# Kernel optimization log

Measured on AMD Instinct MI355X. Metric: run time of the kernel, lower is better.

The kernel has to match this reference:

```python
import jax, jax.numpy as jnp
import numpy as np

N = 1_000_000      # neurons (scaled-up NEURON_COUNT)
E = 20_000_000     # synapses (scaled-up NEURON_COUNT * SYNAPSE_RATIO)
IN = 4096          # input_size
OUT = 4096         # output_size
STEPS = 3


def setup_inputs() -> dict:
    key = jax.random.key(0)
    k1, k2, k3, k4, k5 = jax.random.split(key, 5)
    x = jax.random.normal(k1, (IN,), jnp.float32)
    synapse_src = jax.random.randint(k2, (E,), 0, N)
    synapse_dst = jax.random.randint(k3, (E,), 0, N)
    synapse_weights = jax.random.normal(k4, (E,), jnp.float32)
    neuron_biases = jax.random.normal(k5, (N - IN,), jnp.float32)
    input_indices = jnp.arange(IN)              # first IN neurons are inputs
    output_indices = jnp.arange(N - OUT, N)     # last OUT neurons are outputs
    non_input_indices = jnp.arange(IN, N)       # complement of input_indices
    return {
        "x": x,
        "synapse_weights": synapse_weights,
        "neuron_biases": neuron_biases,
        "synapse_src": synapse_src,
        "synapse_dst": synapse_dst,
        "input_indices": input_indices,
        "output_indices": output_indices,
        "non_input_indices": non_input_indices,
    }


def reference(x, synapse_weights, neuron_biases, synapse_src, synapse_dst,
              input_indices, output_indices, non_input_indices):
    # out_mask[i] True => neuron i is an output (skipped by tanh)
    out_mask = jnp.zeros(N, dtype=bool).at[output_indices].set(True)
    # initial state: zeros with inputs written in
    v = jnp.zeros(N, dtype=x.dtype).at[input_indices].set(x)
    for _ in range(STEPS):
        # per-edge multiply + scatter-add into destination neurons
        msgs = v[synapse_src] * synapse_weights          # [E]
        nxt = jax.ops.segment_sum(msgs, synapse_dst, num_segments=N)  # [N]
        # bias only for non-input neurons
        nxt = nxt.at[non_input_indices].add(neuron_biases)
        # tanh everywhere except output neurons
        v = jnp.where(out_mask, nxt, jnp.tanh(nxt))
    return v[output_indices]
```

## Files before the change

kernel.cpp:

```cpp
#include <hip/hip_runtime.h>

#define THREADS 256
#define BTHREADS 1024
#define SCTHREADS 1024
#define BSHIFT 11
#define BSIZE 2048
#define NBMAX 512
#define PASS_EDGES 8192
#define EPT 8
#define G 4
#define GSHIFT 2
#define ACCSIZE 8192
#define SPLIT 4
#define NPSMAX 640
typedef unsigned int u32;
typedef unsigned short u16;
typedef unsigned long long u64;


__global__ void prep_kernel(const float* __restrict__ x, const float* __restrict__ bias,
                            float* __restrict__ v, float* __restrict__ nxt,
                            int N, int IN) {
    int i = blockIdx.x * THREADS + threadIdx.x;
    if (i >= N) return;
    v[i]   = (i < IN) ? x[i] : 0.0f;
    nxt[i] = (i < IN) ? 0.0f : bias[i - IN];
}

__global__ void finalize0_kernel(float* __restrict__ v, int N, int OUT) {
    int i = blockIdx.x * THREADS + threadIdx.x;
    if (i >= N) return;
    float val = v[i];
    v[i] = (i >= N - OUT) ? val : tanhf(val);
}

__global__ void finalize_fast_kernel(float* __restrict__ nxt, const float* __restrict__ bias,
                                     float* __restrict__ out,
                                     int N, int IN, int OUT) {
    int i = blockIdx.x * THREADS + threadIdx.x;
    if (i >= N) return;
    float val = nxt[i] + (i >= IN ? bias[i - IN] : 0.0f);
    bool isOut = (i >= N - OUT);
    float a = isOut ? val : tanhf(val);
    nxt[i] = a;
    if (out != nullptr && isOut) out[i - (N - OUT)] = a;
}

__global__ void __launch_bounds__(SCTHREADS)
scatter_kernel(const int* __restrict__ src, const int* __restrict__ dst,
               const float* __restrict__ w,
               const float* __restrict__ vA,
               float* __restrict__ vB,
               uint2* __restrict__ e8, u16* __restrict__ dir,
               int E, int IN, int NB, int NP) {
    __shared__ uint2 stage[PASS_EDGES];
    __shared__ u32 hc[NBMAX];
    __shared__ u32 runStart[NBMAX + 1];

    const int tid = threadIdx.x;
    for (int i = tid; i < NBMAX; i += SCTHREADS) hc[i] = 0;
    __syncthreads();

    for (int p = blockIdx.x; p < NP; p += gridDim.x) {
        int ps = p * PASS_EDGES;
        int pe = ps + PASS_EDGES; if (pe > E) pe = E;
        int cntAll = pe - ps;

        int base = ps + tid * EPT;
        u32 pk[EPT]; u32 bk[EPT]; u32 wb[EPT];
        int cnt = 0;
        if (base + EPT <= pe) {
            int4 s0 = *(const int4*)(src + base), s1 = *(const int4*)(src + base + 4);
            int4 d0 = *(const int4*)(dst + base), d1 = *(const int4*)(dst + base + 4);
            float4 w0 = *(const float4*)(w + base), w1 = *(const float4*)(w + base + 4);
            int ss[EPT] = {s0.x, s0.y, s0.z, s0.w, s1.x, s1.y, s1.z, s1.w};
            int dd[EPT] = {d0.x, d0.y, d0.z, d0.w, d1.x, d1.y, d1.z, d1.w};
            float ww[EPT] = {w0.x, w0.y, w0.z, w0.w, w1.x, w1.y, w1.z, w1.w};
            cnt = EPT;
            #pragma unroll
            for (int i = 0; i < EPT; ++i) {
                u32 d = (u32)dd[i];
                bk[i] = d >> BSHIFT;
                pk[i] = (u32)ss[i] | ((d & (BSIZE - 1u)) << 20);
                wb[i] = __float_as_uint(ww[i]);
                if (ss[i] < IN) atomicAdd(&vB[dd[i]], vA[ss[i]] * ww[i]);
            }
        } else {
            for (int i = 0; i < EPT; ++i) {
                int e = base + i;
                if (e < pe) {
                    int s = src[e];
                    u32 d = (u32)dst[e];
                    float wv = w[e];
                    bk[cnt] = d >> BSHIFT;
                    pk[cnt] = (u32)s | ((d & (BSIZE - 1u)) << 20);
                    wb[cnt] = __float_as_uint(wv);
                    if (s < IN) atomicAdd(&vB[d], vA[s] * wv);
                    ++cnt;
                }
            }
        }

        for (int i = 0; i < cnt; ++i) atomicAdd(&hc[bk[i]], 1u);
        __syncthreads();

        if (tid < 64) {
            u32 c[8]; u32 s = 0;
            #pragma unroll
            for (int k = 0; k < 8; ++k) { c[k] = hc[tid * 8 + k]; s += c[k]; }
            u32 inc = s;
            #pragma unroll
            for (int off = 1; off < 64; off <<= 1) {
                u32 t = __shfl_up(inc, off, 64);
                if (tid >= off) inc += t;
            }
            u32 excl = inc - s;
            #pragma unroll
            for (int k = 0; k < 8; ++k) {
                runStart[tid * 8 + k] = excl;
                excl += c[k];
                hc[tid * 8 + k] = 0;
            }
            if (tid == 63) runStart[NBMAX] = excl;
        }
        __syncthreads();

        for (int i = 0; i < cnt; ++i) {
            u32 b = bk[i];
            u32 r = atomicAdd(&hc[b], 1u);
            stage[runStart[b] + r] = make_uint2(pk[i], wb[i]);
        }
        __syncthreads();

        for (int j = tid * 2; j + 1 < cntAll; j += SCTHREADS * 2)
            *(uint4*)(e8 + ps + j) = *(const uint4*)(stage + j);
        if ((cntAll & 1) && tid == 0) e8[ps + cntAll - 1] = stage[cntAll - 1];
        if (tid <= NB) dir[(u32)p * (u32)(NB + 1) + tid] = (u16)runStart[tid];
        if (tid < NBMAX) hc[tid] = 0;
        __syncthreads();
    }
}

__global__ void __launch_bounds__(BTHREADS)
bucket_step_kernel(const uint2* __restrict__ e8, const u16* __restrict__ dir,
                   const float* __restrict__ v_in, float* __restrict__ nxt,
                   int N, int NB, int NP) {
    __shared__ float acc[ACCSIZE];
    __shared__ u16 sb[G + 1][NPSMAX];
    const int tid = threadIdx.x;
    const int gb = blockIdx.x >> 2;
    const int sp = blockIdx.x & 3;

    const int NPS = (NP + SPLIT - 1) / SPLIT;
    const int p0 = sp * NPS;
    int pc = NP - p0; if (pc > NPS) pc = NPS; if (pc < 0) pc = 0;

    const int b0 = gb << GSHIFT;
    for (int idx = tid; idx < pc * (G + 1); idx += BTHREADS) {
        int i = idx / (G + 1), k = idx - i * (G + 1);
        int col = b0 + k; if (col > NB) col = NB;
        sb[k][i] = dir[(u32)(p0 + i) * (u32)(NB + 1) + col];
    }
    for (int i = tid; i < ACCSIZE; i += BTHREADS) acc[i] = 0.0f;
    __syncthreads();

    const int wv = tid >> 6, ln = tid & 63;
    for (int pp = wv; pp < pc; pp += 64) {
        int  jj[4], je[4], eb[4];
        u32  s1[4], s2[4], s3[4];
        bool act[4];
        #pragma unroll
        for (int c = 0; c < 4; ++c) {
            int i = pp + c * 16;
            act[c] = false;
            if (i < pc) {
                u32 a0 = sb[0][i];
                s1[c] = sb[1][i]; s2[c] = sb[2][i]; s3[c] = sb[3][i];
                jj[c] = (int)a0 + ln;
                je[c] = (int)sb[4][i];
                eb[c] = (p0 + i) * PASS_EDGES;
                act[c] = jj[c] < je[c];
            }
        }
        while (act[0] | act[1] | act[2] | act[3]) {
            u64 pv[4];
            #pragma unroll
            for (int c = 0; c < 4; ++c)
                if (act[c]) pv[c] = __builtin_nontemporal_load((const u64*)(e8 + eb[c] + jj[c]));
            float vv[4];
            #pragma unroll
            for (int c = 0; c < 4; ++c)
                if (act[c]) vv[c] = v_in[(u32)pv[c] & 0xFFFFFu];
            #pragma unroll
            for (int c = 0; c < 4; ++c) {
                if (act[c]) {
                    u32 px = (u32)pv[c];
                    u32 j  = (u32)jj[c];
                    u32 r  = (u32)(j >= s1[c]) + (u32)(j >= s2[c]) + (u32)(j >= s3[c]);
                    float pw = __uint_as_float((u32)(pv[c] >> 32));
                    atomicAdd(&acc[(r << BSHIFT) + (px >> 20)], vv[c] * pw);
                    jj[c] += 64;
                    act[c] = jj[c] < je[c];
                }
            }
        }
    }
    __syncthreads();

    int nbase = b0 << BSHIFT;
    for (int j = tid; j < ACCSIZE; j += BTHREADS) {
        int idx = nbase + j;
        if (idx < N) atomicAdd(&nxt[idx], acc[j]);
    }
}


__global__ void edge_kernel(const int* __restrict__ src, const int* __restrict__ dst,
                            const float* __restrict__ w, const float* __restrict__ v,
                            float* __restrict__ nxt, int E) {
    int k = blockIdx.x * THREADS + threadIdx.x;
    int E4 = E >> 2;
    if (k < E4) {
        int4 s = ((const int4*)src)[k];
        int4 d = ((const int4*)dst)[k];
        float4 wv = ((const float4*)w)[k];
        atomicAdd(&nxt[d.x], v[s.x] * wv.x);
        atomicAdd(&nxt[d.y], v[s.y] * wv.y);
        atomicAdd(&nxt[d.z], v[s.z] * wv.z);
        atomicAdd(&nxt[d.w], v[s.w] * wv.w);
    }
    if (k == 0) {
        for (int e = E4 << 2; e < E; ++e)
            atomicAdd(&nxt[dst[e]], v[src[e]] * w[e]);
    }
}

__global__ void finalize_kernel(float* __restrict__ nxt, float* __restrict__ v,
                                const float* __restrict__ bias, float* __restrict__ out,
                                int N, int IN, int OUT) {
    int i = blockIdx.x * THREADS + threadIdx.x;
    if (i >= N) return;
    float val = nxt[i];
    bool isOut = (i >= N - OUT);
    float a = isOut ? val : tanhf(val);
    v[i] = a;
    nxt[i] = (i < IN) ? 0.0f : bias[i - IN];
    if (out != nullptr && isOut) out[i - (N - OUT)] = a;
}


extern "C" void kernel_launch(void* const* d_in, const int* in_sizes, int n_in,
                              void* d_out, int out_size, void* d_ws, size_t ws_size,
                              hipStream_t stream) {
    const float* x    = (const float*)d_in[0];
    const float* w    = (const float*)d_in[1];
    const float* bias = (const float*)d_in[2];
    const int* src = (const int*)d_in[3];
    const int* dst = (const int*)d_in[4];

    const int IN  = in_sizes[0];
    const int E   = in_sizes[1];
    const int N   = IN + in_sizes[2];
    const int OUT = out_size;

    const int NP = (E + PASS_EDGES - 1) / PASS_EDGES;
    const int NB = (N + BSIZE - 1) >> BSHIFT;

    uint2* e8   = (uint2*)d_ws;
    u16*   dir  = (u16*)(e8 + E);
    size_t dirB = (size_t)NP * (size_t)(NB + 1) * sizeof(u16);
    float* vA   = (float*)((char*)dir + ((dirB + 15) & ~(size_t)15));
    float* vB   = vA + N;
    size_t need = (size_t)((char*)(vB + N) - (char*)d_ws);

    int nBlocks = (N + THREADS - 1) / THREADS;

    if (ws_size >= need && N <= (NBMAX << BSHIFT) && NP <= SPLIT * NPSMAX) {
        const int NBG = ((NB + G - 1) >> GSHIFT);
        prep_kernel<<<nBlocks, THREADS, 0, stream>>>(x, bias, vA, vB, N, IN);
        scatter_kernel<<<512, SCTHREADS, 0, stream>>>(
            src, dst, w, vA, vB, e8, dir, E, IN, NB, NP);
        finalize0_kernel<<<nBlocks, THREADS, 0, stream>>>(vB, N, OUT);
        hipMemsetAsync(vA, 0, (size_t)N * sizeof(float), stream);
        bucket_step_kernel<<<NBG * SPLIT, BTHREADS, 0, stream>>>(
            e8, dir, vB, vA, N, NB, NP);
        finalize_fast_kernel<<<nBlocks, THREADS, 0, stream>>>(vA, bias, nullptr, N, IN, OUT);
        hipMemsetAsync(vB, 0, (size_t)N * sizeof(float), stream);
        bucket_step_kernel<<<NBG * SPLIT, BTHREADS, 0, stream>>>(
            e8, dir, vA, vB, N, NB, NP);
        finalize_fast_kernel<<<nBlocks, THREADS, 0, stream>>>(vB, bias, (float*)d_out, N, IN, OUT);
    } else {
        float* v   = (float*)d_ws;
        float* nxt = v + N;
        int eBlocks = ((E >> 2) + THREADS - 1) / THREADS;
        prep_kernel<<<nBlocks, THREADS, 0, stream>>>(x, bias, v, nxt, N, IN);
        for (int step = 0; step < 3; ++step) {
            edge_kernel<<<eBlocks, THREADS, 0, stream>>>(src, dst, w, v, nxt, E);
            float* outp = (step == 2) ? (float*)d_out : nullptr;
            finalize_kernel<<<nBlocks, THREADS, 0, stream>>>(nxt, v, bias, outp, N, IN, OUT);
        }
    }
}
```

Before: 667.1 us.

## Regroup bucketed edges by source tile so consume steps gather from LDS

```diff
diff --git a/kernel.cpp b/kernel.cpp
--- a/kernel.cpp
+++ b/kernel.cpp
@@ -1,15 +1,21 @@
 #include <hip/hip_runtime.h>
 
 #define THREADS 256
-#define BTHREADS 1024
 #define SCTHREADS 1024
 #define BSHIFT 11
 #define BSIZE 2048
 #define NBMAX 512
 #define PASS_EDGES 8192
 #define EPT 8
+#define GSH 13
+#define GRP 8192
 #define G 4
-#define GSHIFT 2
+#define TSH 13
+#define NTILE 128
+#define SLAB 8192
+#define NPQMAX 640
+#define NUMAX 512
+#define BTHREADS 1024
 #define ACCSIZE 8192
 #define SPLIT 4
 #define NPSMAX 640
@@ -46,6 +52,7 @@
     if (out != nullptr && isOut) out[i - (N - OUT)] = a;
 }
 
+
 __global__ void __launch_bounds__(SCTHREADS)
 scatter_kernel(const int* __restrict__ src, const int* __restrict__ dst,
                const float* __restrict__ w,
@@ -53,7 +60,7 @@
                float* __restrict__ vB,
                uint2* __restrict__ e8, u16* __restrict__ dir,
                int E, int IN, int NB, int NP) {
-    __shared__ uint2 stage[PASS_EDGES];
+    __shared__ __align__(16) uint2 stage[PASS_EDGES];
     __shared__ u32 hc[NBMAX];
     __shared__ u32 runStart[NBMAX + 1];
 
@@ -141,6 +148,238 @@
     }
 }
 
+
+__global__ void unitcnt_kernel(const u16* __restrict__ dir1, u32* __restrict__ mc,
+                               int NB, int NP) {
+    __shared__ u32 wsum[4];
+    const int tid = threadIdx.x;
+    const int g = blockIdx.x >> 2, pq = blockIdx.x & 3;
+    const int NPQ = (NP + 3) >> 2;
+    const int p0 = pq * NPQ;
+    int pc = NP - p0; if (pc > NPQ) pc = NPQ; if (pc < 0) pc = 0;
+    int c0 = g * G; if (c0 > NB) c0 = NB;
+    int c1 = g * G + G; if (c1 > NB) c1 = NB;
+    u32 sum = 0;
+    for (int p = tid; p < pc; p += 256) {
+        const u16* row = dir1 + (u32)(p0 + p) * (u32)(NB + 1);
+        sum += (u32)row[c1] - (u32)row[c0];
+    }
+    #pragma unroll
+    for (int off = 32; off; off >>= 1) sum += __shfl_down(sum, off, 64);
+    if ((tid & 63) == 0) wsum[tid >> 6] = sum;
+    __syncthreads();
+    if (tid == 0) mc[blockIdx.x] = wsum[0] + wsum[1] + wsum[2] + wsum[3];
+}
+
+__global__ void unitscan_kernel(const u32* __restrict__ mc, u32* __restrict__ mo,
+                                u32* __restrict__ mr, int NU) {
+    __shared__ u32 s[NUMAX];
+    const int t = threadIdx.x;
+    u32 cnt = (t < NU) ? mc[t] : 0u;
+    u32 pcnt = (cnt + 1u) & ~1u;
+    s[t] = pcnt;
+    __syncthreads();
+    for (int off = 1; off < NUMAX; off <<= 1) {
+        u32 v = (t >= off) ? s[t - off] : 0u;
+        __syncthreads();
+        s[t] += v;
+        __syncthreads();
+    }
+    if (t < NU) mo[t] = s[t] - pcnt;
+    __syncthreads();
+    u32 rows = (cnt + SLAB - 1u) >> 13;
+    s[t] = rows;
+    __syncthreads();
+    for (int off = 1; off < NUMAX; off <<= 1) {
+        u32 v = (t >= off) ? s[t - off] : 0u;
+        __syncthreads();
+        s[t] += v;
+        __syncthreads();
+    }
+    if (t < NU) mr[t] = s[t] - rows;
+}
+
+__global__ void __launch_bounds__(1024)
+regroup_kernel(const uint2* __restrict__ e8, const u16* __restrict__ dir1,
+               const u32* __restrict__ mo, const u32* __restrict__ mr,
+               uint2* __restrict__ e9, u16* __restrict__ dir2,
+               int NB, int NP) {
+    __shared__ __align__(16) uint2 stg[SLAB];
+    __shared__ u16 sb[G + 1][NPQMAX];
+    __shared__ u32 gpfx[NPQMAX + 1];
+    __shared__ u32 scanb[1024];
+    __shared__ u32 hist[NTILE];
+    __shared__ u32 rs2[NTILE + 1];
+    __shared__ int shr[2];
+
+    const int tid = threadIdx.x, wv = tid >> 6, ln = tid & 63;
+    const int g = blockIdx.x >> 2, pq = blockIdx.x & 3;
+    const int b0 = g * G;
+    const int NPQ = (NP + 3) >> 2;
+    const int p0 = pq * NPQ;
+    int pc = NP - p0; if (pc > NPQ) pc = NPQ; if (pc < 0) pc = 0;
+
+    for (int idx = tid; idx < pc * (G + 1); idx += 1024) {
+        int i = idx / (G + 1), k = idx - i * (G + 1);
+        int col = b0 + k; if (col > NB) col = NB;
+        sb[k][i] = dir1[(u32)(p0 + i) * (u32)(NB + 1) + col];
+    }
+    __syncthreads();
+    u32 own = (tid < pc) ? (u32)sb[G][tid] - (u32)sb[0][tid] : 0u;
+    scanb[tid] = own;
+    __syncthreads();
+    for (int off = 1; off < 1024; off <<= 1) {
+        u32 t = (tid >= off) ? scanb[tid - off] : 0u;
+        __syncthreads();
+        scanb[tid] += t;
+        __syncthreads();
+    }
+    if (tid < pc) gpfx[tid] = scanb[tid] - own;
+    if (tid == 0) gpfx[pc] = (pc > 0) ? scanb[pc - 1] : 0u;
+    __syncthreads();
+
+    const u32 cnt = gpfx[pc];
+    const u32 offU = mo[blockIdx.x];
+    const u32 rowB = mr[blockIdx.x];
+    const int nslab = (int)((cnt + SLAB - 1u) >> 13);
+
+    for (int q = 0; q < nslab; ++q) {
+        const u32 lo = (u32)q << 13;
+        u32 hi = lo + SLAB; if (hi > cnt) hi = cnt;
+        if (tid == 0) {
+            int pl = (q == 0) ? 0 : shr[0];
+            while (pl < pc && gpfx[pl + 1] <= lo) ++pl;
+            int ph = pl;
+            while (ph < pc && gpfx[ph] < hi) ++ph;
+            shr[0] = pl; shr[1] = ph;
+        }
+        if (tid < NTILE) hist[tid] = 0;
+        __syncthreads();
+        const int plo = shr[0], phi = shr[1];
+
+        for (int p = plo + wv; p < phi; p += 16) {
+            const u32 gp = gpfx[p], L = gpfx[p + 1] - gp;
+            const u32 s0 = sb[0][p];
+            const size_t eb = (size_t)(p0 + p) * PASS_EDGES + s0;
+            u32 k0 = (lo > gp) ? lo - gp : 0u;
+            u32 k1 = (hi < gp + L) ? hi - gp : L;
+            for (u32 k = k0 + ln; k < k1; k += 64) {
+                u32 pk = e8[eb + k].x;
+                atomicAdd(&hist[(pk & 0xFFFFFu) >> TSH], 1u);
+            }
+        }
+        __syncthreads();
+        if (tid < 64) {
+            u32 c0 = hist[tid * 2], c1 = hist[tid * 2 + 1];
+            u32 s = c0 + c1, inc = s;
+            #pragma unroll
+            for (int off = 1; off < 64; off <<= 1) {
+                u32 t = __shfl_up(inc, off, 64);
+                if (tid >= off) inc += t;
+            }
+            u32 excl = inc - s;
+            rs2[tid * 2] = excl;
+            rs2[tid * 2 + 1] = excl + c0;
+            hist[tid * 2] = 0; hist[tid * 2 + 1] = 0;
+            if (tid == 63) rs2[NTILE] = inc;
+        }
+        __syncthreads();
+        for (int p = plo + wv; p < phi; p += 16) {
+            const u32 gp = gpfx[p], L = gpfx[p + 1] - gp;
+            const u32 s0 = sb[0][p];
+            const u32 b1 = (u32)sb[1][p] - s0, b2 = (u32)sb[2][p] - s0, b3 = (u32)sb[3][p] - s0;
+            const size_t eb = (size_t)(p0 + p) * PASS_EDGES + s0;
+            u32 k0 = (lo > gp) ? lo - gp : 0u;
+            u32 k1 = (hi < gp + L) ? hi - gp : L;
+            for (u32 k = k0 + ln; k < k1; k += 64) {
+                uint2 rec = e8[eb + k];
+                u32 srcg = rec.x & 0xFFFFFu;
+                u32 dl = rec.x >> 20;
+                u32 r = (u32)(k >= b1) + (u32)(k >= b2) + (u32)(k >= b3);
+                u32 tile = srcg >> TSH;
+                u32 rk = atomicAdd(&hist[tile], 1u);
+                stg[rs2[tile] + rk] =
+                    make_uint2((srcg & (GRP - 1u)) | (((r << BSHIFT) | dl) << TSH), rec.y);
+            }
+        }
+        __syncthreads();
+        const u32 m = hi - lo;
+        u64* o64 = (u64*)(e9 + (size_t)offU + ((size_t)q << 13));
+        const u64* s64 = (const u64*)stg;
+        for (u32 j = tid; j < m; j += 1024)
+            __builtin_nontemporal_store(s64[j], o64 + j);
+        if (tid <= NTILE)
+            dir2[(size_t)(rowB + q) * (NTILE + 1) + tid] = (u16)rs2[tid];
+        __syncthreads();
+    }
+}
+
+__global__ void __launch_bounds__(1024)
+consume_kernel(const uint2* __restrict__ e9, const u16* __restrict__ dir2,
+               const u32* __restrict__ mc, const u32* __restrict__ mo,
+               const u32* __restrict__ mr,
+               const float* __restrict__ v_in, float* __restrict__ nxt,
+               int N) {
+    __shared__ float acc[GRP];
+    __shared__ float vt[GRP];
+    __shared__ u32 uoff[4], urow[4], pfx[5];
+
+    const int tid = threadIdx.x, wv = tid >> 6, ln = tid & 63;
+    const int g = blockIdx.x >> 2, sq = blockIdx.x & 3;
+
+    if (tid < 4) {
+        int u = g * 4 + tid;
+        uoff[tid] = mo[u];
+        urow[tid] = mr[u];
+    }
+    __syncthreads();
+    if (tid == 0) {
+        pfx[0] = 0;
+        for (int i = 0; i < 4; ++i) {
+            u32 c = mc[g * 4 + i];
+            pfx[i + 1] = pfx[i] + ((c + SLAB - 1u) >> 13);
+        }
+    }
+    for (int i = tid; i < GRP; i += 1024) acc[i] = 0.0f;
+    __syncthreads();
+    const int tot = (int)pfx[4];
+
+    for (int s = sq * (NTILE / 4); s < (sq + 1) * (NTILE / 4); ++s) {
+        const int vb = s << TSH;
+        if (vb + GRP <= N) {
+            for (int j = tid; j < GRP / 4; j += 1024)
+                *(float4*)&vt[j * 4] = *(const float4*)(v_in + vb + j * 4);
+        } else {
+            for (int j = tid; j < GRP; j += 1024) {
+                int idx = vb + j;
+                vt[j] = (idx < N) ? v_in[idx] : 0.0f;
+            }
+        }
+        __syncthreads();
+        for (int pr = wv; pr < tot; pr += 16) {
+            int u = 0;
+            while (pr >= (int)pfx[u + 1]) ++u;
+            const int q = pr - (int)pfx[u];
+            const u16* row = dir2 + (size_t)(urow[u] + q) * (NTILE + 1) + s;
+            const u32 a = row[0], b = row[1];
+            const uint2* base = e9 + (size_t)uoff[u] + ((size_t)q << 13);
+            for (u32 j = a + ln; j < b; j += 64) {
+                u64 pv = __builtin_nontemporal_load((const u64*)(base + j));
+                u32 px = (u32)pv;
+                float pw = __uint_as_float((u32)(pv >> 32));
+                atomicAdd(&acc[px >> TSH], vt[px & (GRP - 1u)] * pw);
+            }
+        }
+        __syncthreads();
+    }
+    const int nb = g << GSH;
+    for (int j = tid; j < GRP; j += 1024) {
+        int idx = nb + j;
+        if (idx < N) atomicAdd(&nxt[idx], acc[j]);
+    }
+}
+
+
 __global__ void __launch_bounds__(BTHREADS)
 bucket_step_kernel(const uint2* __restrict__ e8, const u16* __restrict__ dir,
                    const float* __restrict__ v_in, float* __restrict__ nxt,
@@ -155,7 +394,7 @@
     const int p0 = sp * NPS;
     int pc = NP - p0; if (pc > NPS) pc = NPS; if (pc < 0) pc = 0;
 
-    const int b0 = gb << GSHIFT;
+    const int b0 = gb << 2;
     for (int idx = tid; idx < pc * (G + 1); idx += BTHREADS) {
         int i = idx / (G + 1), k = idx - i * (G + 1);
         int col = b0 + k; if (col > NB) col = NB;
@@ -265,30 +504,63 @@
 
     const int NP = (E + PASS_EDGES - 1) / PASS_EDGES;
     const int NB = (N + BSIZE - 1) >> BSHIFT;
+    const int NG = (N + GRP - 1) >> GSH;
+    const int NU = NG * 4;
+    const int ROWB = NP + NUMAX + 8;
+
+    int nBlocks = (N + THREADS - 1) / THREADS;
 
     uint2* e8   = (uint2*)d_ws;
-    u16*   dir  = (u16*)(e8 + E);
-    size_t dirB = (size_t)NP * (size_t)(NB + 1) * sizeof(u16);
-    float* vA   = (float*)((char*)dir + ((dirB + 15) & ~(size_t)15));
+    size_t off  = (size_t)E * 8;
+    u16*   dir1 = (u16*)((char*)d_ws + off);
+    off += ((size_t)NP * (NB + 1) * 2 + 15) & ~(size_t)15;
+    uint2* e9   = (uint2*)((char*)d_ws + off);
+    off += (size_t)(E + NUMAX) * 8;
+    u16*   dir2 = (u16*)((char*)d_ws + off);
+    off += ((size_t)ROWB * (NTILE + 1) * 2 + 15) & ~(size_t)15;
+    u32*   mc   = (u32*)((char*)d_ws + off);
+    u32*   mo   = mc + NUMAX;
+    u32*   mr   = mo + NUMAX;
+    off += (size_t)NUMAX * 3 * 4;
+    off = (off + 15) & ~(size_t)15;
+    float* vA   = (float*)((char*)d_ws + off);
     float* vB   = vA + N;
-    size_t need = (size_t)((char*)(vB + N) - (char*)d_ws);
-
-    int nBlocks = (N + THREADS - 1) / THREADS;
-
-    if (ws_size >= need && N <= (NBMAX << BSHIFT) && NP <= SPLIT * NPSMAX) {
-        const int NBG = ((NB + G - 1) >> GSHIFT);
+    size_t needA = off + (size_t)N * 8;
+
+    u16*   dir1B = (u16*)(e8 + E);
+    size_t dirB  = (size_t)NP * (NB + 1) * 2;
+    float* vAB   = (float*)((char*)dir1B + ((dirB + 15) & ~(size_t)15));
+    float* vBB   = vAB + N;
+    size_t needB = (size_t)((char*)(vBB + N) - (char*)d_ws);
+
+    if (ws_size >= needA && N <= (NBMAX << BSHIFT) && NP <= 4 * NPQMAX && NU <= NUMAX) {
         prep_kernel<<<nBlocks, THREADS, 0, stream>>>(x, bias, vA, vB, N, IN);
         scatter_kernel<<<512, SCTHREADS, 0, stream>>>(
-            src, dst, w, vA, vB, e8, dir, E, IN, NB, NP);
+            src, dst, w, vA, vB, e8, dir1, E, IN, NB, NP);
         finalize0_kernel<<<nBlocks, THREADS, 0, stream>>>(vB, N, OUT);
+        unitcnt_kernel<<<NU, 256, 0, stream>>>(dir1, mc, NB, NP);
+        unitscan_kernel<<<1, NUMAX, 0, stream>>>(mc, mo, mr, NU);
+        regroup_kernel<<<NU, 1024, 0, stream>>>(e8, dir1, mo, mr, e9, dir2, NB, NP);
         hipMemsetAsync(vA, 0, (size_t)N * sizeof(float), stream);
-        bucket_step_kernel<<<NBG * SPLIT, BTHREADS, 0, stream>>>(
-            e8, dir, vB, vA, N, NB, NP);
+        consume_kernel<<<NU, 1024, 0, stream>>>(e9, dir2, mc, mo, mr, vB, vA, N);
         finalize_fast_kernel<<<nBlocks, THREADS, 0, stream>>>(vA, bias, nullptr, N, IN, OUT);
         hipMemsetAsync(vB, 0, (size_t)N * sizeof(float), stream);
+        consume_kernel<<<NU, 1024, 0, stream>>>(e9, dir2, mc, mo, mr, vA, vB, N);
+        finalize_fast_kernel<<<nBlocks, THREADS, 0, stream>>>(vB, bias, (float*)d_out, N, IN, OUT);
+    } else if (ws_size >= needB && N <= (NBMAX << BSHIFT) && NP <= SPLIT * NPSMAX) {
+        const int NBG = ((NB + G - 1) >> 2);
+        prep_kernel<<<nBlocks, THREADS, 0, stream>>>(x, bias, vAB, vBB, N, IN);
+        scatter_kernel<<<512, SCTHREADS, 0, stream>>>(
+            src, dst, w, vAB, vBB, e8, dir1B, E, IN, NB, NP);
+        finalize0_kernel<<<nBlocks, THREADS, 0, stream>>>(vBB, N, OUT);
+        hipMemsetAsync(vAB, 0, (size_t)N * sizeof(float), stream);
         bucket_step_kernel<<<NBG * SPLIT, BTHREADS, 0, stream>>>(
-            e8, dir, vA, vB, N, NB, NP);
-        finalize_fast_kernel<<<nBlocks, THREADS, 0, stream>>>(vB, bias, (float*)d_out, N, IN, OUT);
+            e8, dir1B, vBB, vAB, N, NB, NP);
+        finalize_fast_kernel<<<nBlocks, THREADS, 0, stream>>>(vAB, bias, nullptr, N, IN, OUT);
+        hipMemsetAsync(vBB, 0, (size_t)N * sizeof(float), stream);
+        bucket_step_kernel<<<NBG * SPLIT, BTHREADS, 0, stream>>>(
+            e8, dir1B, vAB, vBB, N, NB, NP);
+        finalize_fast_kernel<<<nBlocks, THREADS, 0, stream>>>(vBB, bias, (float*)d_out, N, IN, OUT);
     } else {
         float* v   = (float*)d_ws;
         float* nxt = v + N;
```

New measurement: 667.4 us. No clear change (+0.0%).

## Bucket edges by source tile and gather from shared-memory vertex tile

Applied to the files above, without the earlier changes.

```diff
diff --git a/kernel.cpp b/kernel.cpp
--- a/kernel.cpp
+++ b/kernel.cpp
@@ -1,18 +1,13 @@
 #include <hip/hip_runtime.h>
 
 #define THREADS 256
-#define BTHREADS 1024
 #define SCTHREADS 1024
-#define BSHIFT 11
-#define BSIZE 2048
-#define NBMAX 512
 #define PASS_EDGES 8192
 #define EPT 8
-#define G 4
-#define GSHIFT 2
-#define ACCSIZE 8192
-#define SPLIT 4
-#define NPSMAX 640
+#define TSH 13
+#define TILE 8192
+#define NTIL 128
+#define NPQMAX 640
 typedef unsigned int u32;
 typedef unsigned short u16;
 typedef unsigned long long u64;
@@ -47,18 +42,18 @@
 }
 
 __global__ void __launch_bounds__(SCTHREADS)
-scatter_kernel(const int* __restrict__ src, const int* __restrict__ dst,
-               const float* __restrict__ w,
-               const float* __restrict__ vA,
-               float* __restrict__ vB,
-               uint2* __restrict__ e8, u16* __restrict__ dir,
-               int E, int IN, int NB, int NP) {
-    __shared__ uint2 stage[PASS_EDGES];
-    __shared__ u32 hc[NBMAX];
-    __shared__ u32 runStart[NBMAX + 1];
+scatter3_kernel(const int* __restrict__ src, const int* __restrict__ dst,
+                const float* __restrict__ w,
+                const float* __restrict__ vA,
+                float* __restrict__ vB,
+                uint2* __restrict__ e8, u16* __restrict__ dir,
+                int E, int IN, int NP) {
+    __shared__ __align__(16) uint2 stage[PASS_EDGES];
+    __shared__ u32 hc[NTIL];
+    __shared__ u32 runStart[NTIL + 1];
 
     const int tid = threadIdx.x;
-    for (int i = tid; i < NBMAX; i += SCTHREADS) hc[i] = 0;
+    for (int i = tid; i < NTIL; i += SCTHREADS) hc[i] = 0;
     __syncthreads();
 
     for (int p = blockIdx.x; p < NP; p += gridDim.x) {
@@ -79,23 +74,23 @@
             cnt = EPT;
             #pragma unroll
             for (int i = 0; i < EPT; ++i) {
-                u32 d = (u32)dd[i];
-                bk[i] = d >> BSHIFT;
-                pk[i] = (u32)ss[i] | ((d & (BSIZE - 1u)) << 20);
-                wb[i] = __float_as_uint(ww[i]);
+                u32 s = (u32)ss[i];
+                bk[i] = s >> TSH;
+                pk[i] = (u32)dd[i] | ((s & 0xFFFu) << 20);
+                wb[i] = (__float_as_uint(ww[i]) & ~1u) | ((s >> 12) & 1u);
                 if (ss[i] < IN) atomicAdd(&vB[dd[i]], vA[ss[i]] * ww[i]);
             }
         } else {
             for (int i = 0; i < EPT; ++i) {
                 int e = base + i;
                 if (e < pe) {
-                    int s = src[e];
+                    u32 s = (u32)src[e];
                     u32 d = (u32)dst[e];
                     float wv = w[e];
-                    bk[cnt] = d >> BSHIFT;
-                    pk[cnt] = (u32)s | ((d & (BSIZE - 1u)) << 20);
-                    wb[cnt] = __float_as_uint(wv);
-                    if (s < IN) atomicAdd(&vB[d], vA[s] * wv);
+                    bk[cnt] = s >> TSH;
+                    pk[cnt] = d | ((s & 0xFFFu) << 20);
+                    wb[cnt] = (__float_as_uint(wv) & ~1u) | ((s >> 12) & 1u);
+                    if ((int)s < IN) atomicAdd(&vB[d], vA[s] * wv);
                     ++cnt;
                 }
             }
@@ -105,23 +100,18 @@
         __syncthreads();
 
         if (tid < 64) {
-            u32 c[8]; u32 s = 0;
-            #pragma unroll
-            for (int k = 0; k < 8; ++k) { c[k] = hc[tid * 8 + k]; s += c[k]; }
-            u32 inc = s;
+            u32 c0 = hc[tid * 2], c1 = hc[tid * 2 + 1];
+            u32 s = c0 + c1, inc = s;
             #pragma unroll
             for (int off = 1; off < 64; off <<= 1) {
-                u32 t = __shfl_up(inc, off, 64);
-                if (tid >= off) inc += t;
+                u32 t2 = __shfl_up(inc, off, 64);
+                if (tid >= off) inc += t2;
             }
             u32 excl = inc - s;
-            #pragma unroll
-            for (int k = 0; k < 8; ++k) {
-                runStart[tid * 8 + k] = excl;
-                excl += c[k];
-                hc[tid * 8 + k] = 0;
-            }
-            if (tid == 63) runStart[NBMAX] = excl;
+            runStart[tid * 2] = excl;
+            runStart[tid * 2 + 1] = excl + c0;
+            hc[tid * 2] = 0; hc[tid * 2 + 1] = 0;
+            if (tid == 63) runStart[NTIL] = inc;
         }
         __syncthreads();
 
@@ -132,53 +122,59 @@
         }
         __syncthreads();
 
-        for (int j = tid * 2; j + 1 < cntAll; j += SCTHREADS * 2)
-            *(uint4*)(e8 + ps + j) = *(const uint4*)(stage + j);
-        if ((cntAll & 1) && tid == 0) e8[ps + cntAll - 1] = stage[cntAll - 1];
-        if (tid <= NB) dir[(u32)p * (u32)(NB + 1) + tid] = (u16)runStart[tid];
-        if (tid < NBMAX) hc[tid] = 0;
-        __syncthreads();
-    }
-}
-
-__global__ void __launch_bounds__(BTHREADS)
-bucket_step_kernel(const uint2* __restrict__ e8, const u16* __restrict__ dir,
-                   const float* __restrict__ v_in, float* __restrict__ nxt,
-                   int N, int NB, int NP) {
-    __shared__ float acc[ACCSIZE];
-    __shared__ u16 sb[G + 1][NPSMAX];
-    const int tid = threadIdx.x;
-    const int gb = blockIdx.x >> 2;
-    const int sp = blockIdx.x & 3;
-
-    const int NPS = (NP + SPLIT - 1) / SPLIT;
-    const int p0 = sp * NPS;
-    int pc = NP - p0; if (pc > NPS) pc = NPS; if (pc < 0) pc = 0;
-
-    const int b0 = gb << GSHIFT;
-    for (int idx = tid; idx < pc * (G + 1); idx += BTHREADS) {
-        int i = idx / (G + 1), k = idx - i * (G + 1);
-        int col = b0 + k; if (col > NB) col = NB;
-        sb[k][i] = dir[(u32)(p0 + i) * (u32)(NB + 1) + col];
-    }
-    for (int i = tid; i < ACCSIZE; i += BTHREADS) acc[i] = 0.0f;
+        {
+            const u64* st = (const u64*)stage;
+            u64* o64 = (u64*)e8 + (size_t)ps;
+            for (int j = tid; j < cntAll; j += SCTHREADS)
+                __builtin_nontemporal_store(st[j], o64 + j);
+        }
+        if (tid <= NTIL) dir[(size_t)p * (NTIL + 1) + tid] = (u16)runStart[tid];
+        if (tid < NTIL) hc[tid] = 0;
+        __syncthreads();
+    }
+}
+
+__global__ void __launch_bounds__(1024)
+consume3_kernel(const uint2* __restrict__ e8, const u16* __restrict__ dir,
+                const float* __restrict__ v_in, float* __restrict__ nxt,
+                int N, int NP) {
+    __shared__ float vt[TILE];
+    __shared__ u16 rs[NPQMAX], re[NPQMAX];
+    const int tid = threadIdx.x, wv = tid >> 6, ln = tid & 63;
+    const int t = blockIdx.x >> 2, q = blockIdx.x & 3;
+
+    const int NPQ = (NP + 3) >> 2;
+    const int p0 = q * NPQ;
+    int pc = NP - p0; if (pc > NPQ) pc = NPQ; if (pc < 0) pc = 0;
+
+    for (int i = tid; i < pc; i += 1024) {
+        const u16* row = dir + (size_t)(p0 + i) * (NTIL + 1) + t;
+        rs[i] = row[0];
+        re[i] = row[1];
+    }
+    const int vb = t << TSH;
+    if (vb + TILE <= N) {
+        for (int j = tid; j < TILE / 4; j += 1024)
+            *(float4*)&vt[j * 4] = *(const float4*)(v_in + vb + j * 4);
+    } else {
+        for (int j = tid; j < TILE; j += 1024) {
+            int idx = vb + j;
+            vt[j] = (idx < N) ? v_in[idx] : 0.0f;
+        }
+    }
     __syncthreads();
 
-    const int wv = tid >> 6, ln = tid & 63;
+    const u64* e64 = (const u64*)e8;
     for (int pp = wv; pp < pc; pp += 64) {
-        int  jj[4], je[4], eb[4];
-        u32  s1[4], s2[4], s3[4];
-        bool act[4];
+        int jj[4], je[4]; size_t eb[4]; bool act[4];
         #pragma unroll
         for (int c = 0; c < 4; ++c) {
             int i = pp + c * 16;
             act[c] = false;
             if (i < pc) {
-                u32 a0 = sb[0][i];
-                s1[c] = sb[1][i]; s2[c] = sb[2][i]; s3[c] = sb[3][i];
-                jj[c] = (int)a0 + ln;
-                je[c] = (int)sb[4][i];
-                eb[c] = (p0 + i) * PASS_EDGES;
+                jj[c] = (int)rs[i] + ln;
+                je[c] = (int)re[i];
+                eb[c] = (size_t)(p0 + i) << 13;
                 act[c] = jj[c] < je[c];
             }
         }
@@ -186,31 +182,21 @@
             u64 pv[4];
             #pragma unroll
             for (int c = 0; c < 4; ++c)
-                if (act[c]) pv[c] = __builtin_nontemporal_load((const u64*)(e8 + eb[c] + jj[c]));
-            float vv[4];
-            #pragma unroll
-            for (int c = 0; c < 4; ++c)
-                if (act[c]) vv[c] = v_in[(u32)pv[c] & 0xFFFFFu];
+                if (act[c]) pv[c] = __builtin_nontemporal_load(e64 + eb[c] + jj[c]);
             #pragma unroll
             for (int c = 0; c < 4; ++c) {
                 if (act[c]) {
-                    u32 px = (u32)pv[c];
-                    u32 j  = (u32)jj[c];
-                    u32 r  = (u32)(j >= s1[c]) + (u32)(j >= s2[c]) + (u32)(j >= s3[c]);
-                    float pw = __uint_as_float((u32)(pv[c] >> 32));
-                    atomicAdd(&acc[(r << BSHIFT) + (px >> 20)], vv[c] * pw);
+                    u32 k  = (u32)pv[c];
+                    u32 wb2 = (u32)(pv[c] >> 32);
+                    u32 d  = k & 0xFFFFFu;
+                    u32 s  = (k >> 20) | ((wb2 & 1u) << 12);
+                    float wgt = __uint_as_float(wb2 & ~1u);
+                    atomicAdd(&nxt[d], vt[s] * wgt);
                     jj[c] += 64;
                     act[c] = jj[c] < je[c];
                 }
             }
         }
-    }
-    __syncthreads();
-
-    int nbase = b0 << BSHIFT;
-    for (int j = tid; j < ACCSIZE; j += BTHREADS) {
-        int idx = nbase + j;
-        if (idx < N) atomicAdd(&nxt[idx], acc[j]);
     }
 }
 
@@ -264,30 +250,28 @@
     const int OUT = out_size;
 
     const int NP = (E + PASS_EDGES - 1) / PASS_EDGES;
-    const int NB = (N + BSIZE - 1) >> BSHIFT;
+    const int NT = (N + TILE - 1) >> TSH;
+
+    int nBlocks = (N + THREADS - 1) / THREADS;
 
     uint2* e8   = (uint2*)d_ws;
-    u16*   dir  = (u16*)(e8 + E);
-    size_t dirB = (size_t)NP * (size_t)(NB + 1) * sizeof(u16);
-    float* vA   = (float*)((char*)dir + ((dirB + 15) & ~(size_t)15));
+    size_t off  = (size_t)E * 8;
+    u16*   dir  = (u16*)((char*)d_ws + off);
+    off += ((size_t)NP * (NTIL + 1) * 2 + 15) & ~(size_t)15;
+    float* vA   = (float*)((char*)d_ws + off);
     float* vB   = vA + N;
-    size_t need = (size_t)((char*)(vB + N) - (char*)d_ws);
-
-    int nBlocks = (N + THREADS - 1) / THREADS;
-
-    if (ws_size >= need && N <= (NBMAX << BSHIFT) && NP <= SPLIT * NPSMAX) {
-        const int NBG = ((NB + G - 1) >> GSHIFT);
+    size_t need = off + (size_t)N * 8;
+
+    if (ws_size >= need && N <= (NTIL << TSH) && NP <= 4 * NPQMAX) {
         prep_kernel<<<nBlocks, THREADS, 0, stream>>>(x, bias, vA, vB, N, IN);
-        scatter_kernel<<<512, SCTHREADS, 0, stream>>>(
-            src, dst, w, vA, vB, e8, dir, E, IN, NB, NP);
+        scatter3_kernel<<<512, SCTHREADS, 0, stream>>>(
+            src, dst, w, vA, vB, e8, dir, E, IN, NP);
         finalize0_kernel<<<nBlocks, THREADS, 0, stream>>>(vB, N, OUT);
         hipMemsetAsync(vA, 0, (size_t)N * sizeof(float), stream);
-        bucket_step_kernel<<<NBG * SPLIT, BTHREADS, 0, stream>>>(
-            e8, dir, vB, vA, N, NB, NP);
+        consume3_kernel<<<NT * 4, 1024, 0, stream>>>(e8, dir, vB, vA, N, NP);
         finalize_fast_kernel<<<nBlocks, THREADS, 0, stream>>>(vA, bias, nullptr, N, IN, OUT);
         hipMemsetAsync(vB, 0, (size_t)N * sizeof(float), stream);
-        bucket_step_kernel<<<NBG * SPLIT, BTHREADS, 0, stream>>>(
-            e8, dir, vA, vB, N, NB, NP);
+        consume3_kernel<<<NT * 4, 1024, 0, stream>>>(e8, dir, vA, vB, N, NP);
         finalize_fast_kernel<<<nBlocks, THREADS, 0, stream>>>(vB, bias, (float*)d_out, N, IN, OUT);
     } else {
         float* v   = (float*)d_ws;
```

Result: slower. 2.265 ms (+239.5%).
